# Kernel tuning notes

Measured on AMD Instinct MI355X. Metric: run time of the kernel, lower is better.

The kernel has to match this reference:

```python
import jax, jax.numpy as jnp
import numpy as np

B, S, T, D, H, K, F = 8, 512, 512, 1024, 16, 64, 4096
EPS = 1e-6
NEG = -1e9


def _ln(x, g, b):
    mu = jnp.mean(x, axis=-1, keepdims=True)
    var = jnp.mean(jnp.square(x - mu), axis=-1, keepdims=True)
    return (x - mu) * jax.lax.rsqrt(var + EPS) * g + b


def _mha(q_in, kv_in, wq, bq, wk, bk, wv, bv, wo, bo, mask=None):
    # q_in: [B,S,D], kv_in: [B,T,D]
    q = jnp.einsum('bsd,dhk->bshk', q_in, wq) + bq
    k = jnp.einsum('btd,dhk->bthk', kv_in, wk) + bk
    v = jnp.einsum('btd,dhk->bthk', kv_in, wv) + bv
    scores = jnp.einsum('bshk,bthk->bhst', q, k) / jnp.sqrt(jnp.float32(K))
    if mask is not None:
        scores = jnp.where(mask, scores, NEG)
    attn = jax.nn.softmax(scores, axis=-1)  # [B,H,S,T]
    ctx = jnp.einsum('bhst,bthk->bshk', attn, v)
    out = jnp.einsum('bshk,hkd->bsd', ctx, wo) + bo
    return out, attn


def setup_inputs() -> dict:
    key = jax.random.key(0)
    ks = jax.random.split(key, 24)
    r = lambda i, shape: 0.02 * jax.random.normal(ks[i], shape, dtype=jnp.float32)
    inp = {
        'x': jax.random.normal(ks[0], (B, S, D), dtype=jnp.float32),
        'enc_output': jax.random.normal(ks[1], (B, T, D), dtype=jnp.float32),
        'look_ahead_mask': jnp.tril(jnp.ones((S, S), dtype=bool))[None, None],
        # mha1 (self-attention)
        'wq1': r(2, (D, H, K)), 'bq1': jnp.zeros((H, K), jnp.float32),
        'wk1': r(3, (D, H, K)), 'bk1': jnp.zeros((H, K), jnp.float32),
        'wv1': r(4, (D, H, K)), 'bv1': jnp.zeros((H, K), jnp.float32),
        'wo1': r(5, (H, K, D)), 'bo1': jnp.zeros((D,), jnp.float32),
        # mha2 (cross-attention)
        'wq2': r(6, (D, H, K)), 'bq2': jnp.zeros((H, K), jnp.float32),
        'wk2': r(7, (D, H, K)), 'bk2': jnp.zeros((H, K), jnp.float32),
        'wv2': r(8, (D, H, K)), 'bv2': jnp.zeros((H, K), jnp.float32),
        'wo2': r(9, (H, K, D)), 'bo2': jnp.zeros((D,), jnp.float32),
        # layernorms
        'g1': jnp.ones((D,), jnp.float32), 'be1': jnp.zeros((D,), jnp.float32),
        'g2': jnp.ones((D,), jnp.float32), 'be2': jnp.zeros((D,), jnp.float32),
        'g3': jnp.ones((D,), jnp.float32), 'be3': jnp.zeros((D,), jnp.float32),
        # ffn
        'w_fc1': r(10, (D, F)), 'b_fc1': jnp.zeros((F,), jnp.float32),
        'w_fc2': r(11, (F, D)), 'b_fc2': jnp.zeros((D,), jnp.float32),
    }
    return inp


def reference(x, enc_output, look_ahead_mask,
              wq1, bq1, wk1, bk1, wv1, bv1, wo1, bo1,
              wq2, bq2, wk2, bk2, wv2, bv2, wo2, bo2,
              g1, be1, g2, be2, g3, be3,
              w_fc1, b_fc1, w_fc2, b_fc2):
    attn1, attn_w1 = _mha(x, x, wq1, bq1, wk1, bk1, wv1, bv1, wo1, bo1,
                          mask=look_ahead_mask)
    out1 = _ln(attn1 + x, g1, be1)
    attn2, attn_w2 = _mha(out1, enc_output, wq2, bq2, wk2, bk2, wv2, bv2, wo2, bo2)
    out2 = _ln(attn2 + out1, g2, be2)
    h = jax.nn.relu(jnp.einsum('bsd,df->bsf', out2, w_fc1) + b_fc1)
    out_ffn = jnp.einsum('bsf,fd->bsd', h, w_fc2) + b_fc2
    dec_layer_out = _ln(out_ffn + out2, g3, be3)
    return dec_layer_out, attn_w1, attn_w2
```

## Files before the change

### kernel.cpp

```cpp
#include <hip/hip_runtime.h>

typedef __attribute__((ext_vector_type(4))) float f32x4;
typedef __attribute__((ext_vector_type(8))) __bf16 bf16x8;

__device__ __forceinline__ unsigned short f2b(float f){
  union { float f; unsigned int u; } v; v.f = f;
  unsigned int r = v.u + 0x7FFFu + ((v.u >> 16) & 1u);
  return (unsigned short)(r >> 16);
}
__device__ __forceinline__ float b2f(unsigned short u){
  union { unsigned int u; float f; } v; v.u = ((unsigned int)u) << 16;
  return v.f;
}
__device__ __forceinline__ bool in_is_bf16(const void* g1){
  return ((const unsigned short*)g1)[0] == 0x3F80u;
}

#define GLD16(gp, lp) __builtin_amdgcn_global_load_lds( \
    (const __attribute__((address_space(1))) unsigned int*)(gp), \
    (__attribute__((address_space(3))) unsigned int*)(lp), 16, 0, 0)

__global__ __launch_bounds__(256) void k_fill(float* p, long long n, float v){
  long long i = (long long)blockIdx.x*256 + threadIdx.x;
  long long stride = (long long)gridDim.x*256;
  for(; i < n; i += stride) p[i] = v;
}

struct SmallConv { const void* src[16]; int n[16]; int off[16]; };

__global__ __launch_bounds__(256) void k_small(SmallConv sc, float* dst, const void* g1f){
  bool isb = in_is_bf16(g1f);
  int i = blockIdx.x;
  const void* s = sc.src[i];
  float* d = dst + sc.off[i];
  int n = sc.n[i];
  for(int j = threadIdx.x; j < n; j += 256)
    d[j] = isb ? b2f(((const unsigned short*)s)[j]) : ((const float*)s)[j];
}

__global__ __launch_bounds__(256) void k_act(const void* src, unsigned short* outb,
                                             int n, const void* g1f){
  bool isb = in_is_bf16(g1f);
  int i = blockIdx.x*256 + threadIdx.x;
  int stride = gridDim.x*256;
  for(; i < n; i += stride){
    float v = isb ? b2f(((const unsigned short*)src)[i]) : ((const float*)src)[i];
    outb[i] = f2b(v);
  }
}

struct TW { const void* src[4]; unsigned short* dst[4]; };

__global__ __launch_bounds__(256) void k_transwB(TW tw, int R, int C, const void* g1f){
  bool isb = in_is_bf16(g1f);
  const void* src = tw.src[blockIdx.z];
  unsigned short* dst = tw.dst[blockIdx.z];
  __shared__ float tile[32][33];
  int c0 = blockIdx.x*32, r0 = blockIdx.y*32;
  int tx = threadIdx.x & 31, ty = threadIdx.x >> 5;
  for(int rr = ty; rr < 32; rr += 8){
    size_t o = (size_t)(r0+rr)*C + c0 + tx;
    tile[rr][tx] = isb ? b2f(((const unsigned short*)src)[o]) : ((const float*)src)[o];
  }
  __syncthreads();
  for(int cc = ty; cc < 32; cc += 8)
    dst[(size_t)(c0+cc)*R + r0 + tx] = f2b(tile[tx][cc]);
}

__global__ __launch_bounds__(256) void k_transv(const unsigned short* __restrict__ src,
                                                unsigned short* __restrict__ dst){
  int z = blockIdx.z; int b = z >> 4, h = z & 15;
  __shared__ unsigned short tile[32][33];
  int k0 = blockIdx.x*32, t0 = blockIdx.y*32;
  int tx = threadIdx.x & 31, ty = threadIdx.x >> 5;
  const unsigned short* s = src + (size_t)b*512*1024 + h*64;
  for(int rr = ty; rr < 32; rr += 8)
    tile[rr][tx] = s[(size_t)(t0+rr)*1024 + k0 + tx];
  __syncthreads();
  unsigned short* d = dst + (size_t)z*64*512;
  for(int cc = ty; cc < 32; cc += 8)
    d[(size_t)(k0+cc)*512 + t0 + tx] = tile[tx][cc];
}

template<int EPI>
__global__ __launch_bounds__(256) void k_gemm(
    const unsigned short* __restrict__ A, int lda,
    const unsigned short* __restrict__ Bt, int ldb,
    void* __restrict__ Cout, int ldc,
    const float* __restrict__ bias, const unsigned short* __restrict__ resid, int K)
{
  __shared__ unsigned short As[2][128*32];
  __shared__ unsigned short Bs[2][128*32];
  int tid = threadIdx.x;
  int lane = tid & 63, w = tid >> 6;
  int lr = lane & 15, lg = lane >> 4;
  int m0 = blockIdx.y * 128, n0 = blockIdx.x * 128;
  int wr = w >> 1, wc = w & 1;

  f32x4 acc[4][4];
  #pragma unroll
  for(int m=0;m<4;m++)
    #pragma unroll
    for(int n=0;n<4;n++) acc[m][n] = (f32x4){0.f,0.f,0.f,0.f};

  #pragma unroll
  for(int j=0;j<2;j++){
    int idx = j*256 + tid;
    GLD16(A + (size_t)(m0 + (idx>>2))*lda + (idx&3)*8,
          As[0] + (size_t)(j*256 + (tid & 192))*8);
    GLD16(Bt + (size_t)(n0 + (idx>>2))*ldb + (idx&3)*8,
          Bs[0] + (size_t)(j*256 + (tid & 192))*8);
  }
  __syncthreads();

  int cur = 0;
  for(int k0 = 0; k0 < K; k0 += 32){
    if(k0 + 32 < K){
      #pragma unroll
      for(int j=0;j<2;j++){
        int idx = j*256 + tid;
        GLD16(A + (size_t)(m0 + (idx>>2))*lda + k0 + 32 + (idx&3)*8,
              As[cur^1] + (size_t)(j*256 + (tid & 192))*8);
        GLD16(Bt + (size_t)(n0 + (idx>>2))*ldb + k0 + 32 + (idx&3)*8,
              Bs[cur^1] + (size_t)(j*256 + (tid & 192))*8);
      }
    }
    bf16x8 a[4], b[4];
    #pragma unroll
    for(int m=0;m<4;m++) a[m] = *(const bf16x8*)&As[cur][(wr*64 + m*16 + lr)*32 + lg*8];
    #pragma unroll
    for(int n=0;n<4;n++) b[n] = *(const bf16x8*)&Bs[cur][(wc*64 + n*16 + lr)*32 + lg*8];
    #pragma unroll
    for(int m=0;m<4;m++)
      #pragma unroll
      for(int n=0;n<4;n++)
        acc[m][n] = __builtin_amdgcn_mfma_f32_16x16x32_bf16(a[m], b[n], acc[m][n], 0,0,0);
    __syncthreads();
    cur ^= 1;
  }

  #pragma unroll
  for(int m=0;m<4;m++){
    #pragma unroll
    for(int n=0;n<4;n++){
      int col = n0 + wc*64 + n*16 + lr;
      float bb = bias[col];
      #pragma unroll
      for(int r=0;r<4;r++){
        int row = m0 + wr*64 + m*16 + lg*4 + r;
        size_t o = (size_t)row*ldc + col;
        float v = acc[m][n][r] + bb;
        if constexpr (EPI == 0){
          ((unsigned short*)Cout)[o] = f2b(v);
        } else if constexpr (EPI == 1){
          ((unsigned short*)Cout)[o] = f2b(v > 0.f ? v : 0.f);
        } else if constexpr (EPI == 2){
          ((unsigned short*)Cout)[o] = f2b(v + b2f(resid[o]));
        } else {
          ((float*)Cout)[o] = v + b2f(resid[o]);
        }
      }
    }
  }
}

template<int EPI>
__global__ __launch_bounds__(256) void k_gemm64(
    const unsigned short* __restrict__ A, int lda,
    const unsigned short* __restrict__ Bt, int ldb,
    void* __restrict__ Cout, int ldc,
    const float* __restrict__ bias, const unsigned short* __restrict__ resid, int K)
{
  __shared__ unsigned short As[2][128*32];
  __shared__ unsigned short Bs[2][64*32];
  int tid = threadIdx.x, lane = tid & 63, w = tid >> 6;
  int lr = lane & 15, lg = lane >> 4;
  int m0 = blockIdx.y * 128, n0 = blockIdx.x * 64;

  f32x4 acc[2][4];
  #pragma unroll
  for(int m=0;m<2;m++)
    #pragma unroll
    for(int n=0;n<4;n++) acc[m][n] = (f32x4){0.f,0.f,0.f,0.f};

  #pragma unroll
  for(int j=0;j<2;j++){
    int idx = j*256 + tid;
    GLD16(A + (size_t)(m0 + (idx>>2))*lda + (idx&3)*8,
          As[0] + (size_t)(j*256 + (tid & 192))*8);
  }
  GLD16(Bt + (size_t)(n0 + (tid>>2))*ldb + (tid&3)*8,
        Bs[0] + (size_t)(tid & 192)*8);
  __syncthreads();

  int cur = 0;
  for(int k0 = 0; k0 < K; k0 += 32){
    if(k0 + 32 < K){
      #pragma unroll
      for(int j=0;j<2;j++){
        int idx = j*256 + tid;
        GLD16(A + (size_t)(m0 + (idx>>2))*lda + k0 + 32 + (idx&3)*8,
              As[cur^1] + (size_t)(j*256 + (tid & 192))*8);
      }
      GLD16(Bt + (size_t)(n0 + (tid>>2))*ldb + k0 + 32 + (tid&3)*8,
            Bs[cur^1] + (size_t)(tid & 192)*8);
    }
    bf16x8 a[2], bf[4];
    #pragma unroll
    for(int m=0;m<2;m++) a[m] = *(const bf16x8*)&As[cur][(w*32 + m*16 + lr)*32 + lg*8];
    #pragma unroll
    for(int n=0;n<4;n++) bf[n] = *(const bf16x8*)&Bs[cur][(n*16 + lr)*32 + lg*8];
    #pragma unroll
    for(int m=0;m<2;m++)
      #pragma unroll
      for(int n=0;n<4;n++)
        acc[m][n] = __builtin_amdgcn_mfma_f32_16x16x32_bf16(a[m], bf[n], acc[m][n], 0,0,0);
    __syncthreads();
    cur ^= 1;
  }

  #pragma unroll
  for(int m=0;m<2;m++){
    #pragma unroll
    for(int n=0;n<4;n++){
      int col = n0 + n*16 + lr;
      float bb = bias[col];
      #pragma unroll
      for(int r=0;r<4;r++){
        int row = m0 + w*32 + m*16 + lg*4 + r;
        size_t o = (size_t)row*ldc + col;
        float v = acc[m][n][r] + bb;
        if constexpr (EPI == 0){
          ((unsigned short*)Cout)[o] = f2b(v);
        } else if constexpr (EPI == 1){
          ((unsigned short*)Cout)[o] = f2b(v > 0.f ? v : 0.f);
        } else if constexpr (EPI == 2){
          ((unsigned short*)Cout)[o] = f2b(v + b2f(resid[o]));
        } else {
          ((float*)Cout)[o] = v + b2f(resid[o]);
        }
      }
    }
  }
}

__global__ __launch_bounds__(256) void k_gemmsplit(
    const unsigned short* __restrict__ A, int lda,
    const unsigned short* __restrict__ Bt, int ldb,
    unsigned short* __restrict__ C0, unsigned short* __restrict__ C1,
    unsigned short* __restrict__ C2,
    const float* __restrict__ bias, int K)
{
  __shared__ unsigned short As[2][128*32];
  __shared__ unsigned short Bs[2][128*32];
  int tid = threadIdx.x;
  int lane = tid & 63, w = tid >> 6;
  int lr = lane & 15, lg = lane >> 4;
  int m0 = blockIdx.y * 128, n0 = blockIdx.x * 128;
  int wr = w >> 1, wc = w & 1;
  unsigned short* Cs = (n0 >> 10) == 0 ? C0 : ((n0 >> 10) == 1 ? C1 : C2);
  int nl0 = n0 & 1023;

  f32x4 acc[4][4];
  #pragma unroll
  for(int m=0;m<4;m++)
    #pragma unroll
    for(int n=0;n<4;n++) acc[m][n] = (f32x4){0.f,0.f,0.f,0.f};

  #pragma unroll
  for(int j=0;j<2;j++){
    int idx = j*256 + tid;
    GLD16(A + (size_t)(m0 + (idx>>2))*lda + (idx&3)*8,
          As[0] + (size_t)(j*256 + (tid & 192))*8);
    GLD16(Bt + (size_t)(n0 + (idx>>2))*ldb + (idx&3)*8,
          Bs[0] + (size_t)(j*256 + (tid & 192))*8);
  }
  __syncthreads();

  int cur = 0;
  for(int k0 = 0; k0 < K; k0 += 32){
    if(k0 + 32 < K){
      #pragma unroll
      for(int j=0;j<2;j++){
        int idx = j*256 + tid;
        GLD16(A + (size_t)(m0 + (idx>>2))*lda + k0 + 32 + (idx&3)*8,
              As[cur^1] + (size_t)(j*256 + (tid & 192))*8);
        GLD16(Bt + (size_t)(n0 + (idx>>2))*ldb + k0 + 32 + (idx&3)*8,
              Bs[cur^1] + (size_t)(j*256 + (tid & 192))*8);
      }
    }
    bf16x8 a[4], b[4];
    #pragma unroll
    for(int m=0;m<4;m++) a[m] = *(const bf16x8*)&As[cur][(wr*64 + m*16 + lr)*32 + lg*8];
    #pragma unroll
    for(int n=0;n<4;n++) b[n] = *(const bf16x8*)&Bs[cur][(wc*64 + n*16 + lr)*32 + lg*8];
    #pragma unroll
    for(int m=0;m<4;m++)
      #pragma unroll
      for(int n=0;n<4;n++)
        acc[m][n] = __builtin_amdgcn_mfma_f32_16x16x32_bf16(a[m], b[n], acc[m][n], 0,0,0);
    __syncthreads();
    cur ^= 1;
  }

  #pragma unroll
  for(int m=0;m<4;m++){
    #pragma unroll
    for(int n=0;n<4;n++){
      int colg = n0 + wc*64 + n*16 + lr;
      int coll = nl0 + wc*64 + n*16 + lr;
      float bb = bias[colg];
      #pragma unroll
      for(int r=0;r<4;r++){
        int row = m0 + wr*64 + m*16 + lg*4 + r;
        Cs[(size_t)row*1024 + coll] = f2b(acc[m][n][r] + bb);
      }
    }
  }
}

template<bool CAUSAL>
__global__ __launch_bounds__(256) void k_attnf(
    const unsigned short* __restrict__ Q,
    const unsigned short* __restrict__ Km,
    const unsigned short* __restrict__ Vt,
    float* __restrict__ P,
    unsigned short* __restrict__ C)
{
  int tid = threadIdx.x, lane = tid & 63, w = tid >> 6;
  int lr = lane & 15, lg = lane >> 4;
  int s0 = blockIdx.x * 32;
  int h = blockIdx.y, b = blockIdx.z;
  int z = b*16 + h;
  const unsigned short* Qb = Q + ((size_t)(b*512 + s0))*1024 + h*64;
  const unsigned short* Kb = Km + ((size_t)(b*512))*1024 + h*64;
  float* Pb = P + ((size_t)(z*512 + s0))*512;

  __shared__ unsigned short P_lds[32*520];
  __shared__ float redm[32][4];
  __shared__ float reds[32][4];

  bf16x8 aq[2][2];
  #pragma unroll
  for(int m=0;m<2;m++)
    #pragma unroll
    for(int kk=0;kk<2;kk++)
      aq[m][kk] = *(const bf16x8*)(Qb + (size_t)(m*16 + lr)*1024 + kk*32 + lg*8);

  f32x4 sc[2][8];
  #pragma unroll
  for(int m=0;m<2;m++)
    #pragma unroll
    for(int cb=0;cb<8;cb++) sc[m][cb] = (f32x4){0.f,0.f,0.f,0.f};

  #pragma unroll
  for(int cb=0; cb<8; cb++){
    int col = w*128 + cb*16 + lr;
    #pragma unroll
    for(int kk=0; kk<2; kk++){
      bf16x8 bq = *(const bf16x8*)(Kb + (size_t)col*1024 + kk*32 + lg*8);
      #pragma unroll
      for(int m=0;m<2;m++)
        sc[m][cb] = __builtin_amdgcn_mfma_f32_16x16x32_bf16(aq[m][kk], bq, sc[m][cb], 0,0,0);
    }
  }

  #pragma unroll
  for(int m=0;m<2;m++)
    #pragma unroll
    for(int cb=0;cb<8;cb++)
      #pragma unroll
      for(int r=0;r<4;r++){
        int row_l = m*16 + lg*4 + r;
        int col = w*128 + cb*16 + lr;
        float v = sc[m][cb][r] * 0.125f;
        if(CAUSAL && col > s0 + row_l) v = -1e9f;
        sc[m][cb][r] = v;
      }

  float gmax[2][4];
  #pragma unroll
  for(int m=0;m<2;m++)
    #pragma unroll
    for(int r=0;r<4;r++){
      float pm = -1e30f;
      #pragma unroll
      for(int cb=0;cb<8;cb++) pm = fmaxf(pm, sc[m][cb][r]);
      #pragma unroll
      for(int off=1; off<16; off<<=1) pm = fmaxf(pm, __shfl_xor(pm, off));
      if(lr == 0) redm[m*16 + lg*4 + r][w] = pm;
    }
  __syncthreads();
  #pragma unroll
  for(int m=0;m<2;m++)
    #pragma unroll
    for(int r=0;r<4;r++){
      int row_l = m*16 + lg*4 + r;
      gmax[m][r] = fmaxf(fmaxf(redm[row_l][0], redm[row_l][1]),
                         fmaxf(redm[row_l][2], redm[row_l][3]));
    }
  #pragma unroll
  for(int m=0;m<2;m++)
    #pragma unroll
    for(int r=0;r<4;r++){
      float ps = 0.f;
      #pragma unroll
      for(int cb=0;cb<8;cb++){
        float e = __expf(sc[m][cb][r] - gmax[m][r]);
        sc[m][cb][r] = e;
        ps += e;
      }
      #pragma unroll
      for(int off=1; off<16; off<<=1) ps += __shfl_xor(ps, off);
      if(lr == 0) reds[m*16 + lg*4 + r][w] = ps;
    }
  __syncthreads();
  #pragma unroll
  for(int m=0;m<2;m++)
    #pragma unroll
    for(int r=0;r<4;r++){
      int row_l = m*16 + lg*4 + r;
      float inv = 1.f / (reds[row_l][0] + reds[row_l][1] + reds[row_l][2] + reds[row_l][3]);
      #pragma unroll
      for(int cb=0;cb<8;cb++){
        int col = w*128 + cb*16 + lr;
        float p = sc[m][cb][r] * inv;
        Pb[(size_t)row_l*512 + col] = p;
        P_lds[row_l*520 + col] = f2b(p);
      }
    }
  __syncthreads();

  const unsigned short* Vb = Vt + ((size_t)z*64 + w*16 + lr)*512;
  f32x4 pacc[2];
  pacc[0] = (f32x4){0.f,0.f,0.f,0.f};
  pacc[1] = (f32x4){0.f,0.f,0.f,0.f};
  for(int kk = 0; kk < 16; kk++){
    bf16x8 bfrag = *(const bf16x8*)(Vb + kk*32 + lg*8);
    #pragma unroll
    for(int m=0;m<2;m++){
      bf16x8 afrag = *(const bf16x8*)&P_lds[(m*16 + lr)*520 + kk*32 + lg*8];
      pacc[m] = __builtin_amdgcn_mfma_f32_16x16x32_bf16(afrag, bfrag, pacc[m], 0,0,0);
    }
  }
  #pragma unroll
  for(int m=0;m<2;m++)
    #pragma unroll
    for(int r=0;r<4;r++)
      C[((size_t)(b*512 + s0 + m*16 + lg*4 + r))*1024 + h*64 + w*16 + lr] = f2b(pacc[m][r]);
}

template<int F32IN, int F32OUT>
__global__ __launch_bounds__(256) void k_ln(const void* __restrict__ in,
    const float* __restrict__ g, const float* __restrict__ be,
    void* __restrict__ out)
{
  int row = blockIdx.x, tid = threadIdx.x;
  float v[4];
  if constexpr (F32IN){
    f32x4 u = *(const f32x4*)((const float*)in + (size_t)row*1024 + tid*4);
    v[0]=u[0]; v[1]=u[1]; v[2]=u[2]; v[3]=u[3];
  } else {
    uint2 u = *(const uint2*)((const unsigned short*)in + (size_t)row*1024 + tid*4);
    v[0] = b2f(u.x & 0xFFFF); v[1] = b2f(u.x >> 16);
    v[2] = b2f(u.y & 0xFFFF); v[3] = b2f(u.y >> 16);
  }
  float s = v[0]+v[1]+v[2]+v[3];
  float s2 = v[0]*v[0]+v[1]*v[1]+v[2]*v[2]+v[3]*v[3];
  #pragma unroll
  for(int off=1; off<64; off<<=1){ s += __shfl_xor(s, off); s2 += __shfl_xor(s2, off); }
  __shared__ float red[2][4];
  int w = tid >> 6;
  if((tid & 63) == 0){ red[0][w] = s; red[1][w] = s2; }
  __syncthreads();
  s  = red[0][0]+red[0][1]+red[0][2]+red[0][3];
  s2 = red[1][0]+red[1][1]+red[1][2]+red[1][3];
  float mu = s * (1.f/1024.f);
  float var = s2 * (1.f/1024.f) - mu*mu;
  float rstd = rsqrtf(var + 1e-6f);
  int c = tid*4;
  float y0 = (v[0]-mu)*rstd*g[c+0] + be[c+0];
  float y1 = (v[1]-mu)*rstd*g[c+1] + be[c+1];
  float y2 = (v[2]-mu)*rstd*g[c+2] + be[c+2];
  float y3 = (v[3]-mu)*rstd*g[c+3] + be[c+3];
  if constexpr (F32OUT){
    f32x4 o = {y0, y1, y2, y3};
    *(f32x4*)((float*)out + (size_t)row*1024 + c) = o;
  } else {
    unsigned int o0 = (unsigned int)f2b(y0) | ((unsigned int)f2b(y1) << 16);
    unsigned int o1 = (unsigned int)f2b(y2) | ((unsigned int)f2b(y3) << 16);
    *(uint2*)((unsigned short*)out + (size_t)row*1024 + c) = make_uint2(o0, o1);
  }
}

extern "C" void kernel_launch(void* const* d_in, const int* in_sizes, int n_in,
                              void* d_out, int out_size, void* d_ws, size_t ws_size,
                              hipStream_t stream)
{
  float* out0 = (float*)d_out;

  static const int exp_sizes[29] = {
    4194304, 4194304, 262144,
    1048576, 1024, 1048576, 1024, 1048576, 1024, 1048576, 1024,
    1048576, 1024, 1048576, 1024, 1048576, 1024, 1048576, 1024,
    1024, 1024, 1024, 1024, 1024, 1024,
    4194304, 4096, 4194304, 1024 };
  bool ok = (n_in == 29);
  if(ok) for(int i=0;i<29;i++) if(in_sizes[i] != exp_sizes[i]) { ok = false; break; }
  if(!ok){
    k_fill<<<2048,256,0,stream>>>(out0, (long long)out_size, 100.0f);
    return;
  }
  if(ws_size < (size_t)42074112){
    k_fill<<<2048,256,0,stream>>>(out0, (long long)out_size, 200.0f);
    return;
  }
  bool bigws = ws_size >= (size_t)58851328;

  const void* x_in   = d_in[0];
  const void* enc_in = d_in[1];
  const void* g1f    = d_in[19];

  char* ws = (char*)d_ws;
  float* bias = (float*)(ws);
  unsigned short* SL0 = (unsigned short*)(ws + 131072);
  unsigned short* SL1 = (unsigned short*)(ws + 131072 + 8388608*1);
  unsigned short* SL2 = (unsigned short*)(ws + 131072 + 8388608*2);
  unsigned short* SL3 = (unsigned short*)(ws + 131072 + 8388608*3);
  unsigned short* SL4 = (unsigned short*)(ws + 131072 + 8388608*4);

  float* P1 = out0 + 4194304;
  float* P2 = P1 + 33554432;

  SmallConv scv;
  const int si[16] = {4,6,8,10,12,14,16,18,19,20,21,22,23,24,26,28};
  const int sn[16] = {1024,1024,1024,1024,1024,1024,1024,1024,
                      1024,1024,1024,1024,1024,1024,4096,1024};
  const int so[16] = {0,1024,2048,3072,4096,5120,6144,7168,
                      8192,9216,10240,11264,12288,13312,14336,18432};
  for(int i=0;i<16;i++){ scv.src[i]=d_in[si[i]]; scv.n[i]=sn[i]; scv.off[i]=so[i]; }
  k_small<<<16,256,0,stream>>>(scv, bias, g1f);

  k_act<<<2048,256,0,stream>>>(x_in, SL0, 4194304, g1f);
  {
    TW tw{}; tw.src[0]=d_in[3]; tw.src[1]=d_in[5]; tw.src[2]=d_in[7];
    tw.dst[0]=SL1; tw.dst[1]=SL1+1048576; tw.dst[2]=SL1+2097152;
    k_transwB<<<dim3(32,32,3),256,0,stream>>>(tw, 1024, 1024, g1f);
  }
  k_gemmsplit<<<dim3(24,32),256,0,stream>>>(SL0,1024, SL1,1024, SL2,SL3,SL4, bias+0, 1024);
  k_transv<<<dim3(2,16,128),256,0,stream>>>(SL4, SL1);
  k_attnf<true><<<dim3(16,16,8),256,0,stream>>>(SL2, SL3, SL1, P1, SL4);
  {
    TW tw{}; tw.src[0]=d_in[9]; tw.dst[0]=SL3;
    k_transwB<<<dim3(32,32,1),256,0,stream>>>(tw, 1024, 1024, g1f);
  }
  k_gemm64<2><<<dim3(16,32),256,0,stream>>>(SL4,1024, SL3,1024, SL2,1024, bias+3072, SL0, 1024);
  k_ln<0,0><<<4096,256,0,stream>>>(SL2, bias+8192, bias+9216, SL4);

  k_act<<<2048,256,0,stream>>>(enc_in, SL0, 4194304, g1f);
  {
    TW tw{}; tw.src[0]=d_in[11]; tw.src[1]=d_in[13]; tw.src[2]=d_in[15];
    tw.dst[0]=SL1; tw.dst[1]=SL1+1048576; tw.dst[2]=SL1+2097152;
    k_transwB<<<dim3(32,32,3),256,0,stream>>>(tw, 1024, 1024, g1f);
  }
  k_gemmsplit<<<dim3(16,32),256,0,stream>>>(SL0,1024, SL1+1048576,1024, SL2,SL3,SL3, bias+5120, 1024);
  k_transv<<<dim3(2,16,128),256,0,stream>>>(SL3, SL0);
  k_gemm64<0><<<dim3(16,32),256,0,stream>>>(SL4,1024, SL1,1024, SL3,1024, bias+4096, nullptr, 1024);
  k_attnf<false><<<dim3(16,16,8),256,0,stream>>>(SL3, SL2, SL0, P2, SL1);
  {
    TW tw{}; tw.src[0]=d_in[17]; tw.dst[0]=SL2;
    k_transwB<<<dim3(32,32,1),256,0,stream>>>(tw, 1024, 1024, g1f);
  }
  k_gemm64<2><<<dim3(16,32),256,0,stream>>>(SL1,1024, SL2,1024, SL3,1024, bias+7168, SL4, 1024);
  k_ln<0,0><<<4096,256,0,stream>>>(SL3, bias+10240, bias+11264, SL0);

  {
    TW tw{}; tw.src[0]=d_in[25]; tw.dst[0]=SL1;
    k_transwB<<<dim3(128,32,1),256,0,stream>>>(tw, 1024, 4096, g1f);
  }
  {
    TW tw{}; tw.src[0]=d_in[27]; tw.dst[0]=SL2;
    k_transwB<<<dim3(32,128,1),256,0,stream>>>(tw, 4096, 1024, g1f);
  }
  if(bigws){
    unsigned short* H = SL3;
    k_gemm<1><<<dim3(32,32),256,0,stream>>>(SL0,1024, SL1,1024, H,4096, bias+14336, nullptr, 1024);
    k_gemm64<3><<<dim3(16,32),256,0,stream>>>(H,4096, SL2,4096, out0,1024, bias+18432, SL0, 4096);
    k_ln<1,1><<<4096,256,0,stream>>>(out0, bias+12288, bias+13312, out0);
  } else {
    for(int c=0;c<2;c++){
      unsigned short* arow = SL0 + (size_t)c*2097152;
      float* orow = out0 + (size_t)c*2097152;
      k_gemm<1><<<dim3(32,16),256,0,stream>>>(arow,1024, SL1,1024, SL3,4096, bias+14336, nullptr, 1024);
      k_gemm64<3><<<dim3(16,16),256,0,stream>>>(SL3,4096, SL2,4096, orow,1024, bias+18432, arow, 4096);
      k_ln<1,1><<<2048,256,0,stream>>>(orow, bias+12288, bias+13312, orow);
    }
  }
}
```

Measured before the change: 493.7 us.

## Fuse prep kernels and write V transposed directly from QKV GEMM epilogue

Merges the small-parameter conversion, activation cast and weight transposes (including the output-projection weight) into one prep kernel per attention block, and the two FFN weight transposes into one kernel. The QKV split GEMM now writes the V slice already transposed per (batch, head) with 4-wide stores, which removes the separate k_transv passes. Workspace slots are reassigned so the attention output can overwrite Q in place, which is why __restrict__ is dropped on Q and C. The aim is fewer launches and fewer HBM round trips; the transposed epilogue stores are strided and may coalesce less well.

```diff
diff --git a/kernel.cpp b/kernel.cpp
--- a/kernel.cpp
+++ b/kernel.cpp
@@ -27,59 +27,64 @@
 }
 
 struct SmallConv { const void* src[16]; int n[16]; int off[16]; };
-
-__global__ __launch_bounds__(256) void k_small(SmallConv sc, float* dst, const void* g1f){
+struct TW4 { const void* s[4]; };
+
+template<bool SMALL>
+__global__ __launch_bounds__(256) void k_prepA(SmallConv sc, float* bias,
+    const void* act_in, unsigned short* act_out,
+    TW4 tw, unsigned short* wdst, const void* g1f)
+{
+  __shared__ float tile[32][33];
   bool isb = in_is_bf16(g1f);
-  int i = blockIdx.x;
-  const void* s = sc.src[i];
-  float* d = dst + sc.off[i];
-  int n = sc.n[i];
-  for(int j = threadIdx.x; j < n; j += 256)
-    d[j] = isb ? b2f(((const unsigned short*)s)[j]) : ((const float*)s)[j];
-}
-
-__global__ __launch_bounds__(256) void k_act(const void* src, unsigned short* outb,
-                                             int n, const void* g1f){
+  int bi = blockIdx.x, tid = threadIdx.x;
+  int base = SMALL ? 16 : 0;
+  if(SMALL && bi < 16){
+    const void* s = sc.src[bi];
+    float* d = bias + sc.off[bi];
+    int n = sc.n[bi];
+    for(int j=tid;j<n;j+=256)
+      d[j] = isb ? b2f(((const unsigned short*)s)[j]) : ((const float*)s)[j];
+  } else if(bi < base + 2048){
+    for(int i=(bi-base)*256+tid; i<4194304; i+=2048*256){
+      float v = isb ? b2f(((const unsigned short*)act_in)[i]) : ((const float*)act_in)[i];
+      act_out[i] = f2b(v);
+    }
+  } else {
+    int r = bi - (base + 2048);
+    int wi = r >> 10, rem = r & 1023;
+    int c0 = (rem & 31)*32, r0 = (rem >> 5)*32;
+    const void* src = tw.s[wi];
+    unsigned short* dst = wdst + (size_t)wi*1048576;
+    int tx = tid & 31, ty = tid >> 5;
+    for(int rr=ty; rr<32; rr+=8){
+      size_t o = (size_t)(r0+rr)*1024 + c0 + tx;
+      tile[rr][tx] = isb ? b2f(((const unsigned short*)src)[o]) : ((const float*)src)[o];
+    }
+    __syncthreads();
+    for(int cc=ty; cc<32; cc+=8)
+      dst[(size_t)(c0+cc)*1024 + r0 + tx] = f2b(tile[tx][cc]);
+  }
+}
+
+__global__ __launch_bounds__(256) void k_prep3(
+    const void* fc1, unsigned short* fc1t,
+    const void* fc2, unsigned short* fc2t, const void* g1f)
+{
+  __shared__ float tile[32][33];
   bool isb = in_is_bf16(g1f);
-  int i = blockIdx.x*256 + threadIdx.x;
-  int stride = gridDim.x*256;
-  for(; i < n; i += stride){
-    float v = isb ? b2f(((const unsigned short*)src)[i]) : ((const float*)src)[i];
-    outb[i] = f2b(v);
-  }
-}
-
-struct TW { const void* src[4]; unsigned short* dst[4]; };
-
-__global__ __launch_bounds__(256) void k_transwB(TW tw, int R, int C, const void* g1f){
-  bool isb = in_is_bf16(g1f);
-  const void* src = tw.src[blockIdx.z];
-  unsigned short* dst = tw.dst[blockIdx.z];
-  __shared__ float tile[32][33];
-  int c0 = blockIdx.x*32, r0 = blockIdx.y*32;
-  int tx = threadIdx.x & 31, ty = threadIdx.x >> 5;
-  for(int rr = ty; rr < 32; rr += 8){
+  int bi = blockIdx.x, tid = threadIdx.x;
+  const void* src; unsigned short* dst; int R, C, bx, by;
+  if(bi < 4096){ src = fc1; dst = fc1t; R = 1024; C = 4096; bx = bi & 127; by = bi >> 7; }
+  else { int r = bi - 4096; src = fc2; dst = fc2t; R = 4096; C = 1024; bx = r & 31; by = r >> 5; }
+  int c0 = bx*32, r0 = by*32;
+  int tx = tid & 31, ty = tid >> 5;
+  for(int rr=ty; rr<32; rr+=8){
     size_t o = (size_t)(r0+rr)*C + c0 + tx;
     tile[rr][tx] = isb ? b2f(((const unsigned short*)src)[o]) : ((const float*)src)[o];
   }
   __syncthreads();
-  for(int cc = ty; cc < 32; cc += 8)
+  for(int cc=ty; cc<32; cc+=8)
     dst[(size_t)(c0+cc)*R + r0 + tx] = f2b(tile[tx][cc]);
-}
-
-__global__ __launch_bounds__(256) void k_transv(const unsigned short* __restrict__ src,
-                                                unsigned short* __restrict__ dst){
-  int z = blockIdx.z; int b = z >> 4, h = z & 15;
-  __shared__ unsigned short tile[32][33];
-  int k0 = blockIdx.x*32, t0 = blockIdx.y*32;
-  int tx = threadIdx.x & 31, ty = threadIdx.x >> 5;
-  const unsigned short* s = src + (size_t)b*512*1024 + h*64;
-  for(int rr = ty; rr < 32; rr += 8)
-    tile[rr][tx] = s[(size_t)(t0+rr)*1024 + k0 + tx];
-  __syncthreads();
-  unsigned short* d = dst + (size_t)z*64*512;
-  for(int cc = ty; cc < 32; cc += 8)
-    d[(size_t)(k0+cc)*512 + t0 + tx] = tile[tx][cc];
 }
 
 template<int EPI>
@@ -244,6 +249,7 @@
   }
 }
 
+template<int TSLOT>
 __global__ __launch_bounds__(256) void k_gemmsplit(
     const unsigned short* __restrict__ A, int lda,
     const unsigned short* __restrict__ Bt, int ldb,
@@ -258,7 +264,8 @@
   int lr = lane & 15, lg = lane >> 4;
   int m0 = blockIdx.y * 128, n0 = blockIdx.x * 128;
   int wr = w >> 1, wc = w & 1;
-  unsigned short* Cs = (n0 >> 10) == 0 ? C0 : ((n0 >> 10) == 1 ? C1 : C2);
+  int slot = n0 >> 10;
+  unsigned short* Cs = slot == 0 ? C0 : (slot == 1 ? C1 : C2);
   int nl0 = n0 & 1023;
 
   f32x4 acc[4][4];
@@ -303,17 +310,33 @@
     cur ^= 1;
   }
 
-  #pragma unroll
-  for(int m=0;m<4;m++){
-    #pragma unroll
-    for(int n=0;n<4;n++){
-      int colg = n0 + wc*64 + n*16 + lr;
-      int coll = nl0 + wc*64 + n*16 + lr;
-      float bb = bias[colg];
-      #pragma unroll
-      for(int r=0;r<4;r++){
-        int row = m0 + wr*64 + m*16 + lg*4 + r;
-        Cs[(size_t)row*1024 + coll] = f2b(acc[m][n][r] + bb);
+  if(slot != TSLOT){
+    #pragma unroll
+    for(int m=0;m<4;m++){
+      #pragma unroll
+      for(int n=0;n<4;n++){
+        int coll = nl0 + wc*64 + n*16 + lr;
+        float bb = bias[n0 + wc*64 + n*16 + lr];
+        #pragma unroll
+        for(int r=0;r<4;r++){
+          int row = m0 + wr*64 + m*16 + lg*4 + r;
+          Cs[(size_t)row*1024 + coll] = f2b(acc[m][n][r] + bb);
+        }
+      }
+    }
+  } else {
+    #pragma unroll
+    for(int m=0;m<4;m++){
+      #pragma unroll
+      for(int n=0;n<4;n++){
+        int vcol = nl0 + wc*64 + n*16 + lr;
+        float bb = bias[n0 + wc*64 + n*16 + lr];
+        int rowb = m0 + wr*64 + m*16 + lg*4;
+        int z = (rowb >> 9)*16 + (vcol >> 6);
+        unsigned short tmp[4];
+        #pragma unroll
+        for(int r=0;r<4;r++) tmp[r] = f2b(acc[m][n][r] + bb);
+        *(ushort4*)&Cs[((size_t)(z*64 + (vcol & 63)))*512 + (rowb & 511)] = *(ushort4*)tmp;
       }
     }
   }
@@ -321,11 +344,11 @@
 
 template<bool CAUSAL>
 __global__ __launch_bounds__(256) void k_attnf(
-    const unsigned short* __restrict__ Q,
+    const unsigned short* Q,
     const unsigned short* __restrict__ Km,
     const unsigned short* __restrict__ Vt,
     float* __restrict__ P,
-    unsigned short* __restrict__ C)
+    unsigned short* C)
 {
   int tid = threadIdx.x, lane = tid & 63, w = tid >> 6;
   int lr = lane & 15, lg = lane >> 4;
@@ -511,23 +534,18 @@
     k_fill<<<2048,256,0,stream>>>(out0, (long long)out_size, 100.0f);
     return;
   }
-  if(ws_size < (size_t)42074112){
+  size_t nslots = ws_size > 131072 ? (ws_size - 131072) / 8388608 : 0;
+  if(nslots < 5){
     k_fill<<<2048,256,0,stream>>>(out0, (long long)out_size, 200.0f);
     return;
   }
-  bool bigws = ws_size >= (size_t)58851328;
-
-  const void* x_in   = d_in[0];
-  const void* enc_in = d_in[1];
-  const void* g1f    = d_in[19];
-
+  bool bigws = nslots >= 9;
+
+  const void* g1f = d_in[19];
   char* ws = (char*)d_ws;
   float* bias = (float*)(ws);
-  unsigned short* SL0 = (unsigned short*)(ws + 131072);
-  unsigned short* SL1 = (unsigned short*)(ws + 131072 + 8388608*1);
-  unsigned short* SL2 = (unsigned short*)(ws + 131072 + 8388608*2);
-  unsigned short* SL3 = (unsigned short*)(ws + 131072 + 8388608*3);
-  unsigned short* SL4 = (unsigned short*)(ws + 131072 + 8388608*4);
+  unsigned short* SL[9];
+  for(int i=0;i<9;i++) SL[i] = (unsigned short*)(ws + 131072 + (size_t)i*8388608);
 
   float* P1 = out0 + 4194304;
   float* P2 = P1 + 33554432;
@@ -539,60 +557,44 @@
   const int so[16] = {0,1024,2048,3072,4096,5120,6144,7168,
                       8192,9216,10240,11264,12288,13312,14336,18432};
   for(int i=0;i<16;i++){ scv.src[i]=d_in[si[i]]; scv.n[i]=sn[i]; scv.off[i]=so[i]; }
-  k_small<<<16,256,0,stream>>>(scv, bias, g1f);
-
-  k_act<<<2048,256,0,stream>>>(x_in, SL0, 4194304, g1f);
+
   {
-    TW tw{}; tw.src[0]=d_in[3]; tw.src[1]=d_in[5]; tw.src[2]=d_in[7];
-    tw.dst[0]=SL1; tw.dst[1]=SL1+1048576; tw.dst[2]=SL1+2097152;
-    k_transwB<<<dim3(32,32,3),256,0,stream>>>(tw, 1024, 1024, g1f);
-  }
-  k_gemmsplit<<<dim3(24,32),256,0,stream>>>(SL0,1024, SL1,1024, SL2,SL3,SL4, bias+0, 1024);
-  k_transv<<<dim3(2,16,128),256,0,stream>>>(SL4, SL1);
-  k_attnf<true><<<dim3(16,16,8),256,0,stream>>>(SL2, SL3, SL1, P1, SL4);
+    TW4 tw{}; tw.s[0]=d_in[3]; tw.s[1]=d_in[5]; tw.s[2]=d_in[7]; tw.s[3]=d_in[9];
+    k_prepA<true><<<6160,256,0,stream>>>(scv, bias, d_in[0], SL[0], tw, SL[1], g1f);
+  }
+  k_gemmsplit<2><<<dim3(24,32),256,0,stream>>>(SL[0],1024, SL[1],1024,
+                                               SL[2], SL[3], SL[4], bias+0, 1024);
+  k_attnf<true><<<dim3(16,16,8),256,0,stream>>>(SL[2], SL[3], SL[4], P1, SL[2]);
+  k_gemm64<2><<<dim3(16,32),256,0,stream>>>(SL[2],1024, SL[1]+3145728,1024,
+                                            SL[3],1024, bias+3072, SL[0], 1024);
+  k_ln<0,0><<<4096,256,0,stream>>>(SL[3], bias+8192, bias+9216, SL[4]);
+
   {
-    TW tw{}; tw.src[0]=d_in[9]; tw.dst[0]=SL3;
-    k_transwB<<<dim3(32,32,1),256,0,stream>>>(tw, 1024, 1024, g1f);
-  }
-  k_gemm64<2><<<dim3(16,32),256,0,stream>>>(SL4,1024, SL3,1024, SL2,1024, bias+3072, SL0, 1024);
-  k_ln<0,0><<<4096,256,0,stream>>>(SL2, bias+8192, bias+9216, SL4);
-
-  k_act<<<2048,256,0,stream>>>(enc_in, SL0, 4194304, g1f);
-  {
-    TW tw{}; tw.src[0]=d_in[11]; tw.src[1]=d_in[13]; tw.src[2]=d_in[15];
-    tw.dst[0]=SL1; tw.dst[1]=SL1+1048576; tw.dst[2]=SL1+2097152;
-    k_transwB<<<dim3(32,32,3),256,0,stream>>>(tw, 1024, 1024, g1f);
-  }
-  k_gemmsplit<<<dim3(16,32),256,0,stream>>>(SL0,1024, SL1+1048576,1024, SL2,SL3,SL3, bias+5120, 1024);
-  k_transv<<<dim3(2,16,128),256,0,stream>>>(SL3, SL0);
-  k_gemm64<0><<<dim3(16,32),256,0,stream>>>(SL4,1024, SL1,1024, SL3,1024, bias+4096, nullptr, 1024);
-  k_attnf<false><<<dim3(16,16,8),256,0,stream>>>(SL3, SL2, SL0, P2, SL1);
-  {
-    TW tw{}; tw.src[0]=d_in[17]; tw.dst[0]=SL2;
-    k_transwB<<<dim3(32,32,1),256,0,stream>>>(tw, 1024, 1024, g1f);
-  }
-  k_gemm64<2><<<dim3(16,32),256,0,stream>>>(SL1,1024, SL2,1024, SL3,1024, bias+7168, SL4, 1024);
-  k_ln<0,0><<<4096,256,0,stream>>>(SL3, bias+10240, bias+11264, SL0);
-
-  {
-    TW tw{}; tw.src[0]=d_in[25]; tw.dst[0]=SL1;
-    k_transwB<<<dim3(128,32,1),256,0,stream>>>(tw, 1024, 4096, g1f);
-  }
-  {
-    TW tw{}; tw.src[0]=d_in[27]; tw.dst[0]=SL2;
-    k_transwB<<<dim3(32,128,1),256,0,stream>>>(tw, 4096, 1024, g1f);
-  }
+    TW4 tw{}; tw.s[0]=d_in[11]; tw.s[1]=d_in[13]; tw.s[2]=d_in[15]; tw.s[3]=d_in[17];
+    k_prepA<false><<<6144,256,0,stream>>>(scv, bias, d_in[1], SL[0], tw, SL[1], g1f);
+  }
+  k_gemmsplit<1><<<dim3(16,32),256,0,stream>>>(SL[0],1024, SL[1]+1048576,1024,
+                                               SL[2], SL[3], nullptr, bias+5120, 1024);
+  k_gemm64<0><<<dim3(16,32),256,0,stream>>>(SL[4],1024, SL[1],1024,
+                                            SL[0],1024, bias+4096, nullptr, 1024);
+  k_attnf<false><<<dim3(16,16,8),256,0,stream>>>(SL[0], SL[2], SL[3], P2, SL[0]);
+  k_gemm64<2><<<dim3(16,32),256,0,stream>>>(SL[0],1024, SL[1]+3145728,1024,
+                                            SL[2],1024, bias+7168, SL[4], 1024);
+  k_ln<0,0><<<4096,256,0,stream>>>(SL[2], bias+10240, bias+11264, SL[3]);
+
+  k_prep3<<<8192,256,0,stream>>>(d_in[25], SL[4], d_in[27], SL[0], g1f);
   if(bigws){
-    unsigned short* H = SL3;
-    k_gemm<1><<<dim3(32,32),256,0,stream>>>(SL0,1024, SL1,1024, H,4096, bias+14336, nullptr, 1024);
-    k_gemm64<3><<<dim3(16,32),256,0,stream>>>(H,4096, SL2,4096, out0,1024, bias+18432, SL0, 4096);
+    unsigned short* H = SL[5];
+    k_gemm<1><<<dim3(32,32),256,0,stream>>>(SL[3],1024, SL[4],1024, H,4096, bias+14336, nullptr, 1024);
+    k_gemm64<3><<<dim3(16,32),256,0,stream>>>(H,4096, SL[0],4096, out0,1024, bias+18432, SL[3], 4096);
     k_ln<1,1><<<4096,256,0,stream>>>(out0, bias+12288, bias+13312, out0);
   } else {
+    unsigned short* H = SL[1];
     for(int c=0;c<2;c++){
-      unsigned short* arow = SL0 + (size_t)c*2097152;
+      unsigned short* arow = SL[3] + (size_t)c*2097152;
       float* orow = out0 + (size_t)c*2097152;
-      k_gemm<1><<<dim3(32,16),256,0,stream>>>(arow,1024, SL1,1024, SL3,4096, bias+14336, nullptr, 1024);
-      k_gemm64<3><<<dim3(16,16),256,0,stream>>>(SL3,4096, SL2,4096, orow,1024, bias+18432, arow, 4096);
+      k_gemm<1><<<dim3(32,16),256,0,stream>>>(arow,1024, SL[4],1024, H,4096, bias+14336, nullptr, 1024);
+      k_gemm64<3><<<dim3(16,16),256,0,stream>>>(H,4096, SL[0],4096, orow,1024, bias+18432, arow, 4096);
       k_ln<1,1><<<2048,256,0,stream>>>(orow, bias+12288, bias+13312, orow);
     }
   }
```

Result: faster. 471.6 us (-4.5%).
